# Optimization experiments

Hardware: AMD Instinct MI355X
Metric: run time of the kernel (lower is better)

## Reference

```python
import jax, jax.numpy as jnp
import numpy as np

P = 17  # prediction chunk size
H = 50  # hidden size

def _lstm_cell(x, h, c, Wih, Whh, bih, bhh):
    # torch LSTMCell: gates = x@Wih^T + bih + h@Whh^T + bhh, order i,f,g,o
    g = x @ Wih.T + h @ Whh.T + (bih + bhh)
    i, f, gg, o = jnp.split(g, 4, axis=-1)
    c_new = jax.nn.sigmoid(f) * c + jax.nn.sigmoid(i) * jnp.tanh(gg)
    h_new = jax.nn.sigmoid(o) * jnp.tanh(c_new)
    return h_new, c_new

def setup_inputs() -> dict:
    key = jax.random.key(0)
    ks = jax.random.split(key, 16)
    B, T = 2048, 512
    s = 1.0 / np.sqrt(H)
    u = lambda k, shp: jax.random.uniform(k, shp, jnp.float32, -s, s)
    return {
        "x": jax.random.normal(ks[0], (B, T * P), jnp.float32),
        "W_ih1": u(ks[1], (4 * H, P)),  "W_hh1": u(ks[2], (4 * H, H)),
        "b_ih1": u(ks[3], (4 * H,)),    "b_hh1": u(ks[4], (4 * H,)),
        "W_ih2": u(ks[5], (4 * H, H)),  "W_hh2": u(ks[6], (4 * H, H)),
        "b_ih2": u(ks[7], (4 * H,)),    "b_hh2": u(ks[8], (4 * H,)),
        "W_ih3": u(ks[9], (4 * H, H)),  "W_hh3": u(ks[10], (4 * H, H)),
        "b_ih3": u(ks[11], (4 * H,)),   "b_hh3": u(ks[12], (4 * H,)),
        "W_lin": u(ks[13], (P, H)),     "b_lin": u(ks[14], (P,)),
        "future": 544,
    }

def reference(x, W_ih1, W_hh1, b_ih1, b_hh1, W_ih2, W_hh2, b_ih2, b_hh2,
              W_ih3, W_hh3, b_ih3, b_hh3, W_lin, b_lin, future):
    B = x.shape[0]
    T = x.shape[1] // P
    xs = x.reshape(B, T, P).transpose(1, 0, 2)  # [T, B, P]
    z = jnp.zeros((B, H), jnp.float32)
    init = (z, z, z, z, z, z)

    def cell_stack(state, inp):
        h1, c1, h2, c2, h3, c3 = state
        h1, c1 = _lstm_cell(inp, h1, c1, W_ih1, W_hh1, b_ih1, b_hh1)
        h2, c2 = _lstm_cell(h1, h2, c2, W_ih2, W_hh2, b_ih2, b_hh2)
        h3, c3 = _lstm_cell(h2, h3, c3, W_ih3, W_hh3, b_ih3, b_hh3)
        out = h3 @ W_lin.T + b_lin  # [B, P]
        return (h1, c1, h2, c2, h3, c3), out

    def step(state, xt):
        return cell_stack(state, xt)

    state, outs = jax.lax.scan(step, init, xs)  # outs: [T, B, P]

    n_future = int(future) // P
    if n_future > 0:
        last = outs[-1]

        def fstep(carry, _):
            state, out = carry
            state, out = cell_stack(state, out)
            return (state, out), out

        _, fouts = jax.lax.scan(fstep, (state, last), None, length=n_future)
        outs = jnp.concatenate([outs, fouts], axis=0)  # [T+next, B, P]

    return outs.transpose(1, 0, 2).reshape(B, -1)  # [B, (T+next)*P]
```

## Files before the change

### kernel.cpp

```cpp
#include <hip/hip_runtime.h>
#include <math.h>


#define BATCH    2048
#define PP       17
#define HH       50
#define GG       200
#define MROWS    8
#define NQ       10
#define NTHREADS 512
#define NACTIVE  500
#define NBLOCKS  (BATCH / MROWS)
#define TQ1      7
#define TQ2      10
#define TQ3      10

__device__ __forceinline__ float bf2f(unsigned short u) {
    unsigned int i = ((unsigned int)u) << 16;
    float f; __builtin_memcpy(&f, &i, 4); return f;
}
__device__ __forceinline__ unsigned short f2bf(float f) {
    unsigned int i; __builtin_memcpy(&i, &f, 4);
    return (unsigned short)((i + 0x7fffu + ((i >> 16) & 1u)) >> 16);
}
__device__ __forceinline__ float ldin(const void* p, long i, bool f32) {
    return f32 ? ((const float*)p)[i] : bf2f(((const unsigned short*)p)[i]);
}
__device__ __forceinline__ float fsig(float x) {
    float t = exp2f(-1.44269504089f * x);
    return __builtin_amdgcn_rcpf(1.0f + t);
}
__device__ __forceinline__ float ftanh(float x) {
    float t = exp2f(2.88539008178f * x);
    return 1.0f - 2.0f * __builtin_amdgcn_rcpf(t + 1.0f);
}

extern "C" __global__ void sniff_dtype(const unsigned short* __restrict__ w,
                                       int* __restrict__ flag) {
    int lane = threadIdx.x;
    bool bad = false;
#pragma unroll
    for (int t = 0; t < 4; ++t) {
        float v = bf2f(w[lane * 4 + t]);
        bad |= !(fabsf(v) <= 1.0f);
    }
    unsigned long long m = __ballot(bad);
    if (lane == 0) flag[0] = (m != 0ULL) ? 1 : 0;
}

template <int TQ>
__device__ __forceinline__ void gate_phase(const float* __restrict__ S,
                                           float* __restrict__ gb,
                                           const float (&w)[4][TQ],
                                           int srow, int g4, int q, bool active) {
    if (active) {
        float a[4][8] = {};
        const float4* Sp = (const float4*)(S + (srow + q * TQ) * MROWS);
#pragma unroll
        for (int t = 0; t < TQ; ++t) {
            float4 lo = Sp[2 * t];
            float4 hi = Sp[2 * t + 1];
#pragma unroll
            for (int e = 0; e < 4; ++e) {
                float wv = w[e][t];
                a[e][0] = fmaf(wv, lo.x, a[e][0]); a[e][1] = fmaf(wv, lo.y, a[e][1]);
                a[e][2] = fmaf(wv, lo.z, a[e][2]); a[e][3] = fmaf(wv, lo.w, a[e][3]);
                a[e][4] = fmaf(wv, hi.x, a[e][4]); a[e][5] = fmaf(wv, hi.y, a[e][5]);
                a[e][6] = fmaf(wv, hi.z, a[e][6]); a[e][7] = fmaf(wv, hi.w, a[e][7]);
            }
        }
#pragma unroll
        for (int m = 0; m < 8; ++m) {
            float4 v; v.x = a[0][m]; v.y = a[1][m]; v.z = a[2][m]; v.w = a[3][m];
            *(float4*)(gb + (q * MROWS + m) * GG + 4 * g4) = v;
        }
    }
}

__device__ __forceinline__ void lstm_update(float* __restrict__ S,
                                            const float* __restrict__ gb,
                                            const float* __restrict__ bs,
                                            float& c, int hrow, int tid) {
    int m = tid & 7;
    int j = tid >> 3;
    float ii = bs[j], ff = bs[50 + j], gg = bs[100 + j], oo = bs[150 + j];
#pragma unroll
    for (int q = 0; q < NQ; ++q) {
        const float* b = gb + (q * MROWS + m) * GG;
        ii += b[j]; ff += b[50 + j]; gg += b[100 + j]; oo += b[150 + j];
    }
    float cn = fsig(ff) * c + fsig(ii) * ftanh(gg);
    c = cn;
    S[(hrow + j) * MROWS + m] = fsig(oo) * ftanh(cn);
}

extern "C" __global__ void __launch_bounds__(NTHREADS, 2)
lstm_persistent(const void* __restrict__ x,
                const void* __restrict__ wih1, const void* __restrict__ whh1,
                const void* __restrict__ bih1, const void* __restrict__ bhh1,
                const void* __restrict__ wih2, const void* __restrict__ whh2,
                const void* __restrict__ bih2, const void* __restrict__ bhh2,
                const void* __restrict__ wih3, const void* __restrict__ whh3,
                const void* __restrict__ bih3, const void* __restrict__ bhh3,
                const void* __restrict__ wlin, const void* __restrict__ blin,
                void* __restrict__ out, const int* __restrict__ flag,
                int T, int steps)
{
    const int tid = threadIdx.x;
    __shared__ float S[167 * MROWS];
    __shared__ float gb[NQ * MROWS * GG];
    __shared__ float WLt[50 * PP];
    __shared__ float bs1[GG], bs2[GG], bs3[GG], bl[PP];

    const bool f32 = (flag[0] != 0);

    const int q  = tid / 50;
    const int g4 = tid - q * 50;
    const bool active = (tid < NACTIVE);

    float w1[4][TQ1], w2[4][TQ2], w3[4][TQ3];
    if (active) {
#pragma unroll
        for (int e = 0; e < 4; ++e) {
            const int g = 4 * g4 + e;
#pragma unroll
            for (int t = 0; t < TQ1; ++t) {
                int k = q * TQ1 + t;
                w1[e][t] = (k < 17) ? ldin(wih1, (long)g * 17 + k, f32)
                         : (k < 67) ? ldin(whh1, (long)g * 50 + (k - 17), f32)
                                    : 0.0f;
            }
#pragma unroll
            for (int t = 0; t < TQ2; ++t) {
                int k = q * TQ2 + t;
                w2[e][t] = (k < 50) ? ldin(wih2, (long)g * 50 + k, f32)
                                    : ldin(whh2, (long)g * 50 + (k - 50), f32);
            }
#pragma unroll
            for (int t = 0; t < TQ3; ++t) {
                int k = q * TQ3 + t;
                w3[e][t] = (k < 50) ? ldin(wih3, (long)g * 50 + k, f32)
                                    : ldin(whh3, (long)g * 50 + (k - 50), f32);
            }
        }
    }

    if (tid < GG) {
        bs1[tid] = ldin(bih1, tid, f32) + ldin(bhh1, tid, f32);
        bs2[tid] = ldin(bih2, tid, f32) + ldin(bhh2, tid, f32);
        bs3[tid] = ldin(bih3, tid, f32) + ldin(bhh3, tid, f32);
    } else if (tid < GG + PP) {
        bl[tid - GG] = ldin(blin, tid - GG, f32);
    }
    for (int i = tid; i < 50 * PP; i += NTHREADS) {
        int k = i / PP, p = i - k * PP;
        WLt[i] = ldin(wlin, (long)p * 50 + k, f32);
    }
    for (int i = tid; i < 1200; i += NTHREADS) S[136 + i] = 0.0f;

    const long rowBase = (long)blockIdx.x * MROWS;
    const long xStride = (long)T * PP;
    if (tid < 136) {
        int m = tid / PP, p = tid - (tid / PP) * PP;
        S[p * MROWS + m] = ldin(x, (rowBase + m) * xStride + p, f32);
    }
    float c1 = 0.0f, c2 = 0.0f, c3 = 0.0f;
    __syncthreads();

    const long outStride = (long)steps * PP;
    for (int s = 0; s < steps; ++s) {
        gate_phase<TQ1>(S, gb, w1, 0, g4, q, active);
        __syncthreads();
        if (tid < 400) lstm_update(S, gb, bs1, c1, 17, tid);
        __syncthreads();
        gate_phase<TQ2>(S, gb, w2, 17, g4, q, active);
        __syncthreads();
        if (tid < 400) lstm_update(S, gb, bs2, c2, 67, tid);
        __syncthreads();
        gate_phase<TQ3>(S, gb, w3, 67, g4, q, active);
        __syncthreads();
        if (tid < 400) lstm_update(S, gb, bs3, c3, 117, tid);
        __syncthreads();
        if (tid < 136) {
            int m = tid / PP, p = tid - (tid / PP) * PP;
            float acc = bl[p];
#pragma unroll
            for (int k = 0; k < 50; ++k)
                acc = fmaf(WLt[k * PP + p], S[(117 + k) * MROWS + m], acc);
            long oi = (rowBase + m) * outStride + (long)s * PP + p;
            if (f32) ((float*)out)[oi] = acc;
            else     ((unsigned short*)out)[oi] = f2bf(acc);
            if (s + 1 >= T && s + 1 < steps)
                S[p * MROWS + m] = acc;
        } else if (tid >= 256 && tid < 392) {
            int u = tid - 256;
            int m = u / PP, p = u - (u / PP) * PP;
            if (s + 1 < T)
                S[p * MROWS + m] = ldin(x, (rowBase + m) * xStride + (long)(s + 1) * PP + p, f32);
        }
        __syncthreads();
    }
}

extern "C" void kernel_launch(void* const* d_in, const int* in_sizes, int n_in,
                              void* d_out, int out_size, void* d_ws, size_t ws_size,
                              hipStream_t stream) {
    (void)ws_size; (void)n_in;
    int* flag = (int*)d_ws;

    const int T     = in_sizes[0] / (BATCH * PP);
    const int steps = out_size / (BATCH * PP);

    sniff_dtype<<<1, 64, 0, stream>>>((const unsigned short*)d_in[1], flag);

    lstm_persistent<<<NBLOCKS, NTHREADS, 0, stream>>>(
        d_in[0],
        d_in[1], d_in[2], d_in[3], d_in[4],
        d_in[5], d_in[6], d_in[7], d_in[8],
        d_in[9], d_in[10], d_in[11], d_in[12],
        d_in[13], d_in[14],
        d_out, flag, T, steps);
}
```

Baseline: 3.164 ms.

## Halve rows per block and re-partition gate work for more resident blocks

```diff
diff --git a/kernel.cpp b/kernel.cpp
--- a/kernel.cpp
+++ b/kernel.cpp
@@ -6,14 +6,14 @@
 #define PP       17
 #define HH       50
 #define GG       200
-#define MROWS    8
-#define NQ       10
+#define MROWS    4
+#define NQ       5
 #define NTHREADS 512
 #define NACTIVE  500
 #define NBLOCKS  (BATCH / MROWS)
-#define TQ1      7
-#define TQ2      10
-#define TQ3      10
+#define TQ1      14
+#define TQ2      20
+#define TQ3      20
 
 __device__ __forceinline__ float bf2f(unsigned short u) {
     unsigned int i = ((unsigned int)u) << 16;
@@ -51,28 +51,25 @@
 template <int TQ>
 __device__ __forceinline__ void gate_phase(const float* __restrict__ S,
                                            float* __restrict__ gb,
-                                           const float (&w)[4][TQ],
-                                           int srow, int g4, int q, bool active) {
+                                           const float (&w)[2][TQ],
+                                           int srow, int g2, int q, bool active) {
     if (active) {
-        float a[4][8] = {};
+        float a[2][4] = {};
         const float4* Sp = (const float4*)(S + (srow + q * TQ) * MROWS);
 #pragma unroll
         for (int t = 0; t < TQ; ++t) {
-            float4 lo = Sp[2 * t];
-            float4 hi = Sp[2 * t + 1];
-#pragma unroll
-            for (int e = 0; e < 4; ++e) {
+            float4 ro = Sp[t];
+#pragma unroll
+            for (int e = 0; e < 2; ++e) {
                 float wv = w[e][t];
-                a[e][0] = fmaf(wv, lo.x, a[e][0]); a[e][1] = fmaf(wv, lo.y, a[e][1]);
-                a[e][2] = fmaf(wv, lo.z, a[e][2]); a[e][3] = fmaf(wv, lo.w, a[e][3]);
-                a[e][4] = fmaf(wv, hi.x, a[e][4]); a[e][5] = fmaf(wv, hi.y, a[e][5]);
-                a[e][6] = fmaf(wv, hi.z, a[e][6]); a[e][7] = fmaf(wv, hi.w, a[e][7]);
-            }
-        }
-#pragma unroll
-        for (int m = 0; m < 8; ++m) {
-            float4 v; v.x = a[0][m]; v.y = a[1][m]; v.z = a[2][m]; v.w = a[3][m];
-            *(float4*)(gb + (q * MROWS + m) * GG + 4 * g4) = v;
+                a[e][0] = fmaf(wv, ro.x, a[e][0]); a[e][1] = fmaf(wv, ro.y, a[e][1]);
+                a[e][2] = fmaf(wv, ro.z, a[e][2]); a[e][3] = fmaf(wv, ro.w, a[e][3]);
+            }
+        }
+#pragma unroll
+        for (int m = 0; m < 4; ++m) {
+            float2 v; v.x = a[0][m]; v.y = a[1][m];
+            *(float2*)(gb + (q * MROWS + m) * GG + 2 * g2) = v;
         }
     }
 }
@@ -81,8 +78,8 @@
                                             const float* __restrict__ gb,
                                             const float* __restrict__ bs,
                                             float& c, int hrow, int tid) {
-    int m = tid & 7;
-    int j = tid >> 3;
+    int m = tid & 3;
+    int j = tid >> 2;
     float ii = bs[j], ff = bs[50 + j], gg = bs[100 + j], oo = bs[150 + j];
 #pragma unroll
     for (int q = 0; q < NQ; ++q) {
@@ -94,7 +91,7 @@
     S[(hrow + j) * MROWS + m] = fsig(oo) * ftanh(cn);
 }
 
-extern "C" __global__ void __launch_bounds__(NTHREADS, 2)
+extern "C" __global__ void __launch_bounds__(NTHREADS, 4)
 lstm_persistent(const void* __restrict__ x,
                 const void* __restrict__ wih1, const void* __restrict__ whh1,
                 const void* __restrict__ bih1, const void* __restrict__ bhh1,
@@ -114,15 +111,15 @@
 
     const bool f32 = (flag[0] != 0);
 
-    const int q  = tid / 50;
-    const int g4 = tid - q * 50;
+    const int q  = tid / 100;
+    const int g2 = tid - q * 100;
     const bool active = (tid < NACTIVE);
 
-    float w1[4][TQ1], w2[4][TQ2], w3[4][TQ3];
+    float w1[2][TQ1], w2[2][TQ2], w3[2][TQ3];
     if (active) {
 #pragma unroll
-        for (int e = 0; e < 4; ++e) {
-            const int g = 4 * g4 + e;
+        for (int e = 0; e < 2; ++e) {
+            const int g = 2 * g2 + e;
 #pragma unroll
             for (int t = 0; t < TQ1; ++t) {
                 int k = q * TQ1 + t;
@@ -156,11 +153,11 @@
         int k = i / PP, p = i - k * PP;
         WLt[i] = ldin(wlin, (long)p * 50 + k, f32);
     }
-    for (int i = tid; i < 1200; i += NTHREADS) S[136 + i] = 0.0f;
+    for (int i = tid; i < 150 * MROWS; i += NTHREADS) S[17 * MROWS + i] = 0.0f;
 
     const long rowBase = (long)blockIdx.x * MROWS;
     const long xStride = (long)T * PP;
-    if (tid < 136) {
+    if (tid < PP * MROWS) {
         int m = tid / PP, p = tid - (tid / PP) * PP;
         S[p * MROWS + m] = ldin(x, (rowBase + m) * xStride + p, f32);
     }
@@ -169,19 +166,19 @@
 
     const long outStride = (long)steps * PP;
     for (int s = 0; s < steps; ++s) {
-        gate_phase<TQ1>(S, gb, w1, 0, g4, q, active);
-        __syncthreads();
-        if (tid < 400) lstm_update(S, gb, bs1, c1, 17, tid);
-        __syncthreads();
-        gate_phase<TQ2>(S, gb, w2, 17, g4, q, active);
-        __syncthreads();
-        if (tid < 400) lstm_update(S, gb, bs2, c2, 67, tid);
-        __syncthreads();
-        gate_phase<TQ3>(S, gb, w3, 67, g4, q, active);
-        __syncthreads();
-        if (tid < 400) lstm_update(S, gb, bs3, c3, 117, tid);
-        __syncthreads();
-        if (tid < 136) {
+        gate_phase<TQ1>(S, gb, w1, 0, g2, q, active);
+        __syncthreads();
+        if (tid < 200) lstm_update(S, gb, bs1, c1, 17, tid);
+        __syncthreads();
+        gate_phase<TQ2>(S, gb, w2, 17, g2, q, active);
+        __syncthreads();
+        if (tid < 200) lstm_update(S, gb, bs2, c2, 67, tid);
+        __syncthreads();
+        gate_phase<TQ3>(S, gb, w3, 67, g2, q, active);
+        __syncthreads();
+        if (tid < 200) lstm_update(S, gb, bs3, c3, 117, tid);
+        __syncthreads();
+        if (tid < PP * MROWS) {
             int m = tid / PP, p = tid - (tid / PP) * PP;
             float acc = bl[p];
 #pragma unroll
@@ -192,7 +189,7 @@
             else     ((unsigned short*)out)[oi] = f2bf(acc);
             if (s + 1 >= T && s + 1 < steps)
                 S[p * MROWS + m] = acc;
-        } else if (tid >= 256 && tid < 392) {
+        } else if (tid >= 256 && tid < 256 + PP * MROWS) {
             int u = tid - 256;
             int m = u / PP, p = u - (u / PP) * PP;
             if (s + 1 < T)
```

After: 7.077 ms. +123.7%, slower.
